# Optimization experiments

Measured on AMD Instinct MI355X. Metric: run time of the kernel, lower is better.

Reference implementation:

```python
import jax, jax.numpy as jnp
import numpy as np

# GConvLSTM (torch_geometric_temporal) single step, H=None,C=None -> zeros.
# Each gate g uses two ChebConvs: conv_x_g(X) + conv_h_g(H) + (w_c_g*C for i,f; only i,f,o have w_c) + b_g
# With H=C=0: gate preact = conv_x_g(X) + conv_h_g(0) + b_g. ChebConv(0)=0 only if bias=False;
# torch_geometric_temporal ChebConvs use bias=True by default, so conv_h_g(0) = bias_h_g (a vector).
# We fold conv_h bias into b. Cheb recursion with sym norm, lambda_max=2 default in ChebConv? Actually
# ChebConv requires lambda_max or normalization='sym' default uses lambda_max=2.0 assumption:
# Tx_0 = x; Tx_1 = L_hat @ x where L_hat = -D^-1/2 A D^-1/2 (since L_scaled = L - I = -A_norm for lambda_max=2);
# Tx_k = 2*L_hat@Tx_{k-1} - Tx_{k-2}. out = sum_k Tx_k @ W_k + bias.

MULT = 2
IN_CH = 10
WIDTHS = [8 * MULT, 16 * MULT, 32 * MULT, 76 * MULT]
KS = [2, 3, 4, 5]
NUM_CLASSES = 2
N_NODES = 100000
N_EDGES = 3200000


def _norm_adj(edge_index, n):
    src, dst = edge_index[0], edge_index[1]
    deg = jax.ops.segment_sum(jnp.ones_like(src, dtype=jnp.float32), dst, num_segments=n)
    dinv = jnp.where(deg > 0, jax.lax.rsqrt(jnp.maximum(deg, 1.0)), 0.0)
    w = dinv[src] * dinv[dst]  # [E]
    return src, dst, w


def _lhat_mul(x, src, dst, w, n):
    # L_hat @ x = -A_norm @ x  (lambda_max=2, sym norm, no self loops added in scaled L beyond -I cancel)
    msg = x[src] * w[:, None]  # [E,F]
    agg = jax.ops.segment_sum(msg, dst, num_segments=n)
    return -agg


def cheb_conv(x, Ws, b, src, dst, w, n):
    # Ws: [K, F_in, F_out]
    K = Ws.shape[0]
    Tx0 = x
    out = Tx0 @ Ws[0]
    if K > 1:
        Tx1 = _lhat_mul(Tx0, src, dst, w, n)
        out = out + Tx1 @ Ws[1]
        for k in range(2, K):
            Tx2 = 2.0 * _lhat_mul(Tx1, src, dst, w, n) - Tx0
            out = out + Tx2 @ Ws[k]
            Tx0, Tx1 = Tx1, Tx2
    return out + b


def gconv_lstm_step(x, params, src, dst, w, n):
    # params: dict with per-gate Wx,Wh (cheb weights), bx,bh, b, and w_ci,w_cf,w_co
    def conv_pair(g):
        cx = cheb_conv(x, params[f'Wx_{g}'], params[f'bx_{g}'], src, dst, w, n)
        # H = 0 => conv_h contributes only its bias
        return cx + params[f'bh_{g}'] + params[f'b_{g}']
    # C = 0 => peephole terms w_c*C vanish
    i = jax.nn.sigmoid(conv_pair('i'))
    f = jax.nn.sigmoid(conv_pair('f'))
    c = i * jnp.tanh(conv_pair('c'))
    o = jax.nn.sigmoid(conv_pair('o'))
    h = o * jnp.tanh(c)
    return h


def _make_layer_params(key, f_in, f_out, K):
    p = {}
    ks = jax.random.split(key, 16)
    scale = 1.0 / np.sqrt(f_in * K)
    for gi, g in enumerate(['i', 'f', 'c', 'o']):
        p[f'Wx_{g}'] = jax.random.normal(ks[4 * gi], (K, f_in, f_out), jnp.float32) * scale
        p[f'bx_{g}'] = jnp.zeros((f_out,), jnp.float32)
        p[f'bh_{g}'] = jnp.zeros((f_out,), jnp.float32)
        p[f'b_{g}'] = jnp.zeros((f_out,), jnp.float32)
    return p


def setup_inputs() -> dict:
    key = jax.random.key(0)
    kx, ke, kp, kl = jax.random.split(key, 4)
    x = jax.random.normal(kx, (N_NODES, IN_CH), jnp.float32)
    edge_index = jax.random.randint(ke, (2, N_EDGES), 0, N_NODES, dtype=jnp.int64)
    layer_keys = jax.random.split(kp, 4)
    params = []
    f_in = IN_CH
    for li, (f_out, K) in enumerate(zip(WIDTHS, KS)):
        params.append(_make_layer_params(layer_keys[li], f_in, f_out, K))
        f_in = f_out
    flat = {}
    for li, p in enumerate(params):
        for k, v in p.items():
            flat[f'l{li}_{k}'] = v
    kw, kb = jax.random.split(kl)
    flat['lin_W'] = jax.random.normal(kw, (WIDTHS[-1], NUM_CLASSES), jnp.float32) * (1.0 / np.sqrt(WIDTHS[-1]))
    flat['lin_b'] = jnp.zeros((NUM_CLASSES,), jnp.float32)
    return {'x': x, 'edge_index': edge_index, **flat}


_GATE_KEYS = [f'{pre}_{g}' for g in ['i', 'f', 'c', 'o'] for pre in ['Wx', 'bx', 'bh', 'b']]


def _forward(x, edge_index, params_by_layer, lin_W, lin_b):
    n = x.shape[0]
    src, dst, w = _norm_adj(edge_index, n)
    h = x
    for p in params_by_layer:
        h = gconv_lstm_step(h, p, src, dst, w, n)
        h = jax.nn.relu(h)  # dropout: eval mode -> identity
    logits = h @ lin_W + lin_b
    return jax.nn.softmax(logits, axis=-1)


def reference(x, edge_index,
              l0_Wx_i, l0_bx_i, l0_bh_i, l0_b_i, l0_Wx_f, l0_bx_f, l0_bh_f, l0_b_f, l0_Wx_c, l0_bx_c, l0_bh_c, l0_b_c, l0_Wx_o, l0_bx_o, l0_bh_o, l0_b_o,
              l1_Wx_i, l1_bx_i, l1_bh_i, l1_b_i, l1_Wx_f, l1_bx_f, l1_bh_f, l1_b_f, l1_Wx_c, l1_bx_c, l1_bh_c, l1_b_c, l1_Wx_o, l1_bx_o, l1_bh_o, l1_b_o,
              l2_Wx_i, l2_bx_i, l2_bh_i, l2_b_i, l2_Wx_f, l2_bx_f, l2_bh_f, l2_b_f, l2_Wx_c, l2_bx_c, l2_bh_c, l2_b_c, l2_Wx_o, l2_bx_o, l2_bh_o, l2_b_o,
              l3_Wx_i, l3_bx_i, l3_bh_i, l3_b_i, l3_Wx_f, l3_bx_f, l3_bh_f, l3_b_f, l3_Wx_c, l3_bx_c, l3_bh_c, l3_b_c, l3_Wx_o, l3_bx_o, l3_bh_o, l3_b_o,
              lin_W, lin_b):
    loc = locals()
    params_by_layer = []
    for li in range(4):
        params_by_layer.append({k: loc[f'l{li}_{k}'] for k in _GATE_KEYS})
    return _forward(x, edge_index, params_by_layer, lin_W, lin_b)
```

## Files before the change

### kernel.cpp

```cpp
#include <hip/hip_runtime.h>


#define IN_CH 10
typedef unsigned short u16;
typedef unsigned long long u64;
typedef short bf16x8 __attribute__((ext_vector_type(8)));
typedef float f32x4 __attribute__((ext_vector_type(4)));

struct __align__(8) Edge { int s; float w; };

__device__ __forceinline__ float bf2f(u16 u) { return __uint_as_float(((unsigned)u) << 16); }
__device__ __forceinline__ float lo16f(unsigned v) { return __uint_as_float(v << 16); }
__device__ __forceinline__ float hi16f(unsigned v) { return __uint_as_float(v & 0xffff0000u); }
__device__ __forceinline__ u16 f2bf(float f) {
    unsigned x = __float_as_uint(f);
    return (u16)((x + 0x7fff + ((x >> 16) & 1)) >> 16);
}
__device__ __forceinline__ float ldv(const float* p) { return *p; }
__device__ __forceinline__ float ldv(const u16* p) { return bf2f(*p); }
__device__ __forceinline__ void stv(float* p, float v) { *p = v; }
__device__ __forceinline__ void stv(u16* p, float v) { *p = f2bf(v); }

__device__ __forceinline__ void gload16(const u16* g, u16* l) {
    __builtin_amdgcn_global_load_lds(
        (const __attribute__((address_space(1))) unsigned*)(const void*)g,
        (__attribute__((address_space(3))) unsigned*)(void*)l, 16, 0, 0);
}


__global__ void k_count(const int* __restrict__ dst, int* __restrict__ cnt, int e) {
    int i = blockIdx.x * 256 + threadIdx.x;
    if (i < e) atomicAdd(&cnt[dst[i]], 1);
}

__global__ void k_dinv(const int* __restrict__ cnt, float* __restrict__ dinv, int n) {
    int i = blockIdx.x * 256 + threadIdx.x;
    if (i < n) dinv[i] = cnt[i] > 0 ? rsqrtf((float)cnt[i]) : 0.f;
}


__global__ void k_bsum(const int* __restrict__ cnt, int* __restrict__ bsum, int n) {
    __shared__ int red[256];
    int t = threadIdx.x;
    int idx = blockIdx.x * 1024 + t * 4;
    int s = 0;
#pragma unroll
    for (int j = 0; j < 4; j++) s += (idx + j < n) ? cnt[idx + j] : 0;
    red[t] = s;
    __syncthreads();
    for (int off = 128; off > 0; off >>= 1) {
        if (t < off) red[t] += red[t + off];
        __syncthreads();
    }
    if (t == 0) bsum[blockIdx.x] = red[0];
}

__global__ __launch_bounds__(1024) void k_bscan(const int* __restrict__ bsum,
                                                int* __restrict__ boff,
                                                int* __restrict__ total_out, int B) {
    __shared__ int sh[1024];
    int t = threadIdx.x;
    int v = t < B ? bsum[t] : 0;
    sh[t] = v;
    __syncthreads();
    for (int off = 1; off < 1024; off <<= 1) {
        int x = (t >= off) ? sh[t - off] : 0;
        __syncthreads();
        sh[t] += x;
        __syncthreads();
    }
    if (t < B) boff[t] = sh[t] - v;
    if (t == B - 1) *total_out = sh[t];
}

__global__ void k_write(const int* __restrict__ cnt, const int* __restrict__ boff,
                        int* __restrict__ row_ptr, int* __restrict__ cursor, int n) {
    __shared__ int tsum[256];
    int t = threadIdx.x;
    int idx = blockIdx.x * 1024 + t * 4;
    int c[4];
    int s = 0;
#pragma unroll
    for (int j = 0; j < 4; j++) {
        c[j] = (idx + j < n) ? cnt[idx + j] : 0;
        s += c[j];
    }
    tsum[t] = s;
    __syncthreads();
    for (int off = 1; off < 256; off <<= 1) {
        int x = (t >= off) ? tsum[t - off] : 0;
        __syncthreads();
        tsum[t] += x;
        __syncthreads();
    }
    int run = boff[blockIdx.x] + tsum[t] - s;
#pragma unroll
    for (int j = 0; j < 4; j++) {
        if (idx + j < n) {
            row_ptr[idx + j] = run;
            cursor[idx + j] = run;
            run += c[j];
        }
    }
}

__global__ void k_fill(const int* __restrict__ src, const int* __restrict__ dst,
                       const float* __restrict__ dinv, int* __restrict__ cursor,
                       Edge* __restrict__ ed, int e, int dlo, int dhi) {
    int i = blockIdx.x * 256 + threadIdx.x;
    if (i >= e) return;
    int d = dst[i];
    if (d < dlo || d >= dhi) return;
    int s = src[i];
    int pos = atomicAdd(&cursor[d], 1);
    float w = dinv[s] * dinv[d];
    u64 v = (u64)(unsigned)s | ((u64)__float_as_uint(w) << 32);
    *(u64*)&ed[pos] = v;
}


template <int F>
__global__ void k_spmv(const u16* __restrict__ X, const u16* __restrict__ Tprev,
                       u16* __restrict__ Tout, const int* __restrict__ row_ptr,
                       const Edge* __restrict__ ed, int n, float scale) {
    int lane = threadIdx.x;
    int node = blockIdx.x * blockDim.y + threadIdx.y;
    if (node >= n) return;
    int lo = row_ptr[node], hi = row_ptr[node + 1];
    const u16* Xc = X + 2 * lane;
    float a0[4] = {0.f, 0.f, 0.f, 0.f};
    float a1[4] = {0.f, 0.f, 0.f, 0.f};
    int e = lo;
    for (; e + 8 <= hi; e += 8) {
        Edge q[8];
#pragma unroll
        for (int j = 0; j < 8; j++) q[j] = ed[e + j];
        unsigned v[8];
#pragma unroll
        for (int j = 0; j < 8; j++)
            v[j] = *(const unsigned*)(Xc + (size_t)q[j].s * F);
#pragma unroll
        for (int j = 0; j < 8; j++) {
            a0[j & 3] = fmaf(q[j].w, lo16f(v[j]), a0[j & 3]);
            a1[j & 3] = fmaf(q[j].w, hi16f(v[j]), a1[j & 3]);
        }
    }
    for (; e + 4 <= hi; e += 4) {
        Edge q[4];
#pragma unroll
        for (int j = 0; j < 4; j++) q[j] = ed[e + j];
        unsigned v[4];
#pragma unroll
        for (int j = 0; j < 4; j++)
            v[j] = *(const unsigned*)(Xc + (size_t)q[j].s * F);
#pragma unroll
        for (int j = 0; j < 4; j++) {
            a0[j] = fmaf(q[j].w, lo16f(v[j]), a0[j]);
            a1[j] = fmaf(q[j].w, hi16f(v[j]), a1[j]);
        }
    }
    for (; e < hi; e++) {
        Edge q = ed[e];
        unsigned v = *(const unsigned*)(Xc + (size_t)q.s * F);
        a0[0] = fmaf(q.w, lo16f(v), a0[0]);
        a1[0] = fmaf(q.w, hi16f(v), a1[0]);
    }
    float v0 = -scale * ((a0[0] + a0[1]) + (a0[2] + a0[3]));
    float v1 = -scale * ((a1[0] + a1[1]) + (a1[2] + a1[3]));
    if (Tprev) {
        unsigned pv = *(const unsigned*)(Tprev + (size_t)node * F + 2 * lane);
        v0 -= lo16f(pv);
        v1 -= hi16f(pv);
    }
    *(unsigned*)(Tout + (size_t)node * F + 2 * lane) =
        (unsigned)f2bf(v0) | ((unsigned)f2bf(v1) << 16);
}

struct TP { const void* p[5]; };

template <typename ST, int FIN, int K>
__global__ __launch_bounds__(256) void k_chebgate(TP tp, const float* __restrict__ Wp,
                                                  const float* __restrict__ b4,
                                                  ST* __restrict__ H, int n, int F,
                                                  int F4pad) {
    __shared__ float As[FIN][68];
    __shared__ float Ws[FIN][128];
    const int tid = threadIdx.x;
    const int fx = tid & 31, ry = tid >> 5;
    const int row0 = blockIdx.y * 64;
    const int f0 = blockIdx.x * 32;
    const int f = f0 + fx;

    float acc[8][3];
    const float4 bv = *(const float4*)&b4[(size_t)f * 4];
#pragma unroll
    for (int r = 0; r < 8; r++) { acc[r][0] = bv.x; acc[r][1] = bv.y; acc[r][2] = bv.z; }

#pragma unroll
    for (int t = 0; t < K; t++) {
        const ST* T = (const ST*)tp.p[t];
        for (int idx = tid; idx < 64 * FIN; idx += 256) {
            int r = idx / FIN, a = idx - r * FIN;
            int rr = row0 + r;
            if (rr >= n) rr = n - 1;
            As[a][r] = ldv(&T[(size_t)rr * FIN + a]);
        }
        const float* Wt = Wp + (size_t)t * FIN * F4pad + (size_t)f0 * 4;
        for (int idx = tid; idx < FIN * 128; idx += 256) {
            int aa = idx >> 7, c = idx & 127;
            Ws[aa][c] = Wt[(size_t)aa * F4pad + c];
        }
        __syncthreads();
#pragma unroll 2
        for (int a = 0; a < FIN; a++) {
            const float4 w = *(const float4*)&Ws[a][fx * 4];
            const float4 x0 = *(const float4*)&As[a][ry * 8];
            const float4 x1 = *(const float4*)&As[a][ry * 8 + 4];
            const float xr[8] = {x0.x, x0.y, x0.z, x0.w, x1.x, x1.y, x1.z, x1.w};
#pragma unroll
            for (int r = 0; r < 8; r++) {
                acc[r][0] = fmaf(xr[r], w.x, acc[r][0]);
                acc[r][1] = fmaf(xr[r], w.y, acc[r][1]);
                acc[r][2] = fmaf(xr[r], w.z, acc[r][2]);
            }
        }
        __syncthreads();
    }

    if (f < F) {
#pragma unroll
        for (int r = 0; r < 8; r++) {
            int row = row0 + ry * 8 + r;
            if (row < n) {
                float gi = 1.f / (1.f + __expf(-acc[r][0]));
                float go = 1.f / (1.f + __expf(-acc[r][2]));
                float c = gi * tanhf(acc[r][1]);
                float h = go * tanhf(c);
                stv(&H[(size_t)row * F + f], fmaxf(h, 0.f));
            }
        }
    }
}


template <int FIN, int K, int NT, int FPAD>
__global__ __launch_bounds__(256) void k_chebgate_mfma2(TP tp, const u16* __restrict__ Bp,
                                                        const float* __restrict__ b3,
                                                        u16* __restrict__ H, int n, int F,
                                                        int Hstride) {
    constexpr int NIT = K * FIN / 32;
    constexpr int CPR = FIN / 8;
    constexpr int CSH = (CPR == 8) ? 3 : 2;
    constexpr int PANEL = 128 * FIN;
    constexpr int IPT = (128 * CPR) / 256;
    __shared__ __align__(16) u16 Alds[K * PANEL];

    const int tid = threadIdx.x;
    const int xb = blockIdx.x;
    const int wv = tid >> 6, lane = tid & 63;
    const int ln = lane & 15, lk = lane >> 4;
    const size_t panel_g = (size_t)xb * 128 * FIN;

#pragma unroll
    for (int t = 0; t < K; t++) {
        const u16* g = (const u16*)tp.p[t] + panel_g;
#pragma unroll
        for (int i = 0; i < IPT; i++) {
            int j0 = wv * (IPT * 64) + i * 64;
            int j = j0 + lane;
            int row = j >> CSH, c = j & (CPR - 1);
            int sc = (j & ~(CPR - 1)) | (c ^ (row & (CPR - 1)));
            gload16(g + (size_t)sc * 8, Alds + (size_t)t * PANEL + (size_t)j0 * 8);
        }
    }
    __syncthreads();

    const int r0 = xb * 128 + wv * 32;
    const u16* Bl = Bp + (size_t)lane * 8;

#pragma unroll 1
    for (int yb = 0; yb < NT; yb++) {
        f32x4 acc[2][2][3];
#pragma unroll
        for (int rt = 0; rt < 2; rt++)
#pragma unroll
            for (int s = 0; s < 2; s++)
#pragma unroll
                for (int g = 0; g < 3; g++) acc[rt][s][g] = (f32x4){0.f, 0.f, 0.f, 0.f};

#pragma unroll
        for (int it = 0; it < NIT; it++) {
            const int k0 = it * 32;
            const int t = k0 / FIN;
            const int a0 = k0 % FIN;
            bf16x8 af[2];
#pragma unroll
            for (int rt = 0; rt < 2; rt++) {
                int lrow = wv * 32 + rt * 16 + ln;
                int kc = (a0 >> 3) + lk;
                int kcs = kc ^ (lrow & (CPR - 1));
                af[rt] = *(const bf16x8*)(Alds + (size_t)t * PANEL + (size_t)lrow * FIN + kcs * 8);
            }
#pragma unroll
            for (int s = 0; s < 2; s++)
#pragma unroll
                for (int g = 0; g < 3; g++) {
                    int fi = (yb * NIT + it) * 6 + s * 3 + g;
                    bf16x8 bf = *(const bf16x8*)(Bl + (size_t)fi * 512);
#pragma unroll
                    for (int rt = 0; rt < 2; rt++)
                        acc[rt][s][g] = __builtin_amdgcn_mfma_f32_16x16x32_bf16(
                            af[rt], bf, acc[rt][s][g], 0, 0, 0);
                }
        }

        const int f0 = yb * 32;
#pragma unroll
        for (int s = 0; s < 2; s++) {
            int fcol = f0 + s * 16 + ln;
            if (fcol >= F) continue;
            float bi = b3[0 * FPAD + fcol];
            float bc = b3[1 * FPAD + fcol];
            float bo = b3[2 * FPAD + fcol];
#pragma unroll
            for (int rt = 0; rt < 2; rt++) {
#pragma unroll
                for (int reg = 0; reg < 4; reg++) {
                    int row = r0 + rt * 16 + lk * 4 + reg;
                    if (row < n) {
                        float gi = 1.f / (1.f + __expf(-(acc[rt][s][0][reg] + bi)));
                        float go = 1.f / (1.f + __expf(-(acc[rt][s][2][reg] + bo)));
                        float c = gi * tanhf(acc[rt][s][1][reg] + bc);
                        float h = go * tanhf(c);
                        H[(size_t)row * Hstride + fcol] = f2bf(fmaxf(h, 0.f));
                    }
                }
            }
        }
    }
}


template <int FIN, int K, int NT, int FPAD>
__global__ __launch_bounds__(256) void k_chebgate_mfma_fused2(
    TP tp, const u16* __restrict__ Bp, const float* __restrict__ b3,
    const float* __restrict__ W2, float* __restrict__ part, int n, int F) {
    constexpr int NIT = K * FIN / 32;
    constexpr int CPR = FIN / 8;
    constexpr int CSH = (CPR == 8) ? 3 : 2;
    constexpr int PANEL = 128 * FIN;
    constexpr int IPT = (128 * CPR) / 256;
    __shared__ __align__(16) u16 Alds[K * PANEL];

    const int tid = threadIdx.x;
    const int xb = blockIdx.x;
    const int wv = tid >> 6, lane = tid & 63;
    const int ln = lane & 15, lk = lane >> 4;
    const size_t panel_g = (size_t)xb * 128 * FIN;

#pragma unroll
    for (int t = 0; t < K; t++) {
        const u16* g = (const u16*)tp.p[t] + panel_g;
#pragma unroll
        for (int i = 0; i < IPT; i++) {
            int j0 = wv * (IPT * 64) + i * 64;
            int j = j0 + lane;
            int row = j >> CSH, c = j & (CPR - 1);
            int sc = (j & ~(CPR - 1)) | (c ^ (row & (CPR - 1)));
            gload16(g + (size_t)sc * 8, Alds + (size_t)t * PANEL + (size_t)j0 * 8);
        }
    }
    __syncthreads();

    const int r0 = xb * 128 + wv * 32;
    const u16* Bl = Bp + (size_t)lane * 8;

#pragma unroll 1
    for (int yb = 0; yb < NT; yb++) {
        f32x4 acc[2][2][3];
#pragma unroll
        for (int rt = 0; rt < 2; rt++)
#pragma unroll
            for (int s = 0; s < 2; s++)
#pragma unroll
                for (int g = 0; g < 3; g++) acc[rt][s][g] = (f32x4){0.f, 0.f, 0.f, 0.f};

#pragma unroll
        for (int it = 0; it < NIT; it++) {
            const int k0 = it * 32;
            const int t = k0 / FIN;
            const int a0 = k0 % FIN;
            bf16x8 af[2];
#pragma unroll
            for (int rt = 0; rt < 2; rt++) {
                int lrow = wv * 32 + rt * 16 + ln;
                int kc = (a0 >> 3) + lk;
                int kcs = kc ^ (lrow & (CPR - 1));
                af[rt] = *(const bf16x8*)(Alds + (size_t)t * PANEL + (size_t)lrow * FIN + kcs * 8);
            }
#pragma unroll
            for (int s = 0; s < 2; s++)
#pragma unroll
                for (int g = 0; g < 3; g++) {
                    int fi = (yb * NIT + it) * 6 + s * 3 + g;
                    bf16x8 bf = *(const bf16x8*)(Bl + (size_t)fi * 512);
#pragma unroll
                    for (int rt = 0; rt < 2; rt++)
                        acc[rt][s][g] = __builtin_amdgcn_mfma_f32_16x16x32_bf16(
                            af[rt], bf, acc[rt][s][g], 0, 0, 0);
                }
        }

        const int f0 = yb * 32;
        float p0[2][4], p1[2][4];
#pragma unroll
        for (int rt = 0; rt < 2; rt++)
#pragma unroll
            for (int reg = 0; reg < 4; reg++) { p0[rt][reg] = 0.f; p1[rt][reg] = 0.f; }

#pragma unroll
        for (int s = 0; s < 2; s++) {
            int fcol = f0 + s * 16 + ln;
            float w20 = fcol < F ? W2[fcol * 2 + 0] : 0.f;
            float w21 = fcol < F ? W2[fcol * 2 + 1] : 0.f;
            float bi = b3[0 * FPAD + fcol];
            float bc = b3[1 * FPAD + fcol];
            float bo = b3[2 * FPAD + fcol];
#pragma unroll
            for (int rt = 0; rt < 2; rt++) {
#pragma unroll
                for (int reg = 0; reg < 4; reg++) {
                    float gi = 1.f / (1.f + __expf(-(acc[rt][s][0][reg] + bi)));
                    float go = 1.f / (1.f + __expf(-(acc[rt][s][2][reg] + bo)));
                    float c = gi * tanhf(acc[rt][s][1][reg] + bc);
                    float h = fmaxf(go * tanhf(c), 0.f);
                    p0[rt][reg] = fmaf(h, w20, p0[rt][reg]);
                    p1[rt][reg] = fmaf(h, w21, p1[rt][reg]);
                }
            }
        }

#pragma unroll
        for (int rt = 0; rt < 2; rt++) {
#pragma unroll
            for (int reg = 0; reg < 4; reg++) {
                float v0 = p0[rt][reg], v1 = p1[rt][reg];
#pragma unroll
                for (int m = 1; m <= 8; m <<= 1) {
                    v0 += __shfl_xor(v0, m);
                    v1 += __shfl_xor(v1, m);
                }
                p0[rt][reg] = v0;
                p1[rt][reg] = v1;
            }
        }

        if (ln == 0) {
#pragma unroll
            for (int rt = 0; rt < 2; rt++) {
#pragma unroll
                for (int reg = 0; reg < 4; reg++) {
                    int row = r0 + rt * 16 + lk * 4 + reg;
                    if (row < n) {
                        float* pp = part + ((size_t)yb * n + row) * 2;
                        pp[0] = p0[rt][reg];
                        pp[1] = p1[rt][reg];
                    }
                }
            }
        }
    }
}

__global__ void k_smax(const float* __restrict__ part, const float* __restrict__ b,
                       float* __restrict__ out, int n, int ntiles) {
    int i = blockIdx.x * 256 + threadIdx.x;
    if (i >= n) return;
    float l0 = b[0], l1 = b[1];
    for (int t = 0; t < ntiles; t++) {
        const float* pp = part + ((size_t)t * n + i) * 2;
        l0 += pp[0];
        l1 += pp[1];
    }
    float m = fmaxf(l0, l1);
    float e0 = __expf(l0 - m), e1 = __expf(l1 - m);
    float s = 1.f / (e0 + e1);
    out[(size_t)i * 2 + 0] = e0 * s;
    out[(size_t)i * 2 + 1] = e1 * s;
}


__global__ void k_pack_w(const float* __restrict__ Wi, const float* __restrict__ Wc,
                         const float* __restrict__ Wo, float* __restrict__ Wp,
                         int KFIN, int F, int F4pad) {
    int idx = blockIdx.x * 256 + threadIdx.x;
    int tot = KFIN * F4pad;
    if (idx >= tot) return;
    int c = idx % F4pad;
    int ka = idx / F4pad;
    int f = c >> 2, g = c & 3;
    float v = 0.f;
    if (g < 3 && f < F) {
        const float* Wg = (g == 0) ? Wi : ((g == 1) ? Wc : Wo);
        v = Wg[(size_t)ka * F + f];
    }
    Wp[idx] = v;
}

__global__ void k_pack_b(const float* __restrict__ bxi, const float* __restrict__ bhi,
                         const float* __restrict__ bi, const float* __restrict__ bxc,
                         const float* __restrict__ bhc, const float* __restrict__ bc,
                         const float* __restrict__ bxo, const float* __restrict__ bho,
                         const float* __restrict__ bo, float* __restrict__ b4,
                         int F, int F4pad) {
    int idx = blockIdx.x * 256 + threadIdx.x;
    if (idx >= F4pad) return;
    int f = idx >> 2, g = idx & 3;
    float v = 0.f;
    if (g < 3 && f < F) {
        if (g == 0) v = bxi[f] + bhi[f] + bi[f];
        else if (g == 1) v = bxc[f] + bhc[f] + bc[f];
        else v = bxo[f] + bho[f] + bo[f];
    }
    b4[idx] = v;
}

__global__ void k_pack_wf(const float* __restrict__ Wi, const float* __restrict__ Wc,
                          const float* __restrict__ Wo, u16* __restrict__ Bp,
                          int NIT, int Fin, int F, int NT) {
    int idx = blockIdx.x * 256 + threadIdx.x;
    int tot = NT * NIT * 6 * 512;
    if (idx >= tot) return;
    int frag = idx >> 9;
    int r = idx & 511;
    int lane = r >> 3, j = r & 7;
    int lk = lane >> 4, ln = lane & 15;
    int yb = frag / (NIT * 6);
    int q = frag % (NIT * 6);
    int it = q / 6, sg = q % 6;
    int s = sg / 3, g = sg % 3;
    int fcol = yb * 32 + s * 16 + ln;
    int k = it * 32 + lk * 8 + j;
    int t = k / Fin, a = k % Fin;
    float v = 0.f;
    if (fcol < F) {
        const float* Wg = (g == 0) ? Wi : ((g == 1) ? Wc : Wo);
        v = Wg[((size_t)t * Fin + a) * F + fcol];
    }
    Bp[idx] = f2bf(v);
}

__global__ void k_pack_b3(const float* __restrict__ bxi, const float* __restrict__ bhi,
                          const float* __restrict__ bi, const float* __restrict__ bxc,
                          const float* __restrict__ bhc, const float* __restrict__ bc,
                          const float* __restrict__ bxo, const float* __restrict__ bho,
                          const float* __restrict__ bo, float* __restrict__ b3,
                          int F, int FPAD) {
    int idx = blockIdx.x * 256 + threadIdx.x;
    if (idx >= 3 * FPAD) return;
    int g = idx / FPAD, f = idx % FPAD;
    float v = 0.f;
    if (f < F) {
        if (g == 0) v = bxi[f] + bhi[f] + bi[f];
        else if (g == 1) v = bxc[f] + bhc[f] + bc[f];
        else v = bxo[f] + bho[f] + bo[f];
    }
    b3[idx] = v;
}

__global__ void k_cvt(const float* __restrict__ x, u16* __restrict__ y, int n) {
    int i = blockIdx.x * 256 + threadIdx.x;
    if (i < n) y[i] = f2bf(x[i]);
}


static inline size_t al(size_t x) { return (x + 255) & ~(size_t)255; }

extern "C" void kernel_launch(void* const* d_in, const int* in_sizes, int n_in,
                              void* d_out, int out_size, void* d_ws, size_t ws_size,
                              hipStream_t stream) {
    const float* X0 = (const float*)d_in[0];
    const int* ei = (const int*)d_in[1];
    const int N = in_sizes[0] / IN_CH;
    const int E = in_sizes[1] / 2;
    const int* src = ei;
    const int* dst = ei + E;

    char* p = (char*)d_ws;
    size_t off = 0;
    auto carve = [&](size_t bytes) -> char* { char* r = p + off; off += al(bytes); return r; };
    int* row_ptr  = (int*)carve((size_t)(N + 1) * 4);
    int* cnt      = (int*)carve((size_t)N * 4);
    int* cursor   = (int*)carve((size_t)N * 4);
    float* dinv   = (float*)carve((size_t)N * 4);
    int* bsum     = (int*)carve((size_t)1024 * 4);
    int* boff     = (int*)carve((size_t)1024 * 4);
    Edge* edges   = (Edge*)carve((size_t)E * 8);
    const size_t S64 = al((size_t)N * 64 * 2);
    char* bufA    = carve(5 * S64);
    char* bufB    = carve((size_t)N * 304);
    float* Wp     = (float*)carve((size_t)48 * 128 * 4);
    float* b4     = (float*)carve((size_t)128 * 4);
    u16* Wt       = (u16*)carve((size_t)480 * 320 * 2);
    float* b3     = (float*)carve((size_t)480 * 4);
    (void)ws_size;

    u16* X0c  = (u16*)bufA;
    u16* T0_1 = (u16*)(bufA + al((size_t)N * 20));
    u16* H0   = (u16*)(bufA + S64);
    u16* T1_1 = (u16*)(bufA + S64 + al((size_t)N * 32));
    u16* T1_2 = (u16*)(bufA + S64 + 2 * al((size_t)N * 32));
    u16* L2T[4];
    for (int t = 0; t < 4; t++) L2T[t] = (u16*)(bufB + t * al((size_t)N * 64));
    u16* L3T[5];
    for (int t = 0; t < 5; t++) L3T[t] = (u16*)(bufA + t * S64);
    float* part = (float*)bufB;

    int gE = (E + 255) / 256, gN = (N + 255) / 256;
    int B = (N + 1023) / 1024;
    hipMemsetAsync(cnt, 0, (size_t)N * 4, stream);
    k_count<<<gE, 256, 0, stream>>>(dst, cnt, E);
    k_dinv<<<gN, 256, 0, stream>>>(cnt, dinv, N);
    k_bsum<<<B, 256, 0, stream>>>(cnt, bsum, N);
    k_bscan<<<1, 1024, 0, stream>>>(bsum, boff, row_ptr + N, B);
    k_write<<<B, 256, 0, stream>>>(cnt, boff, row_ptr, cursor, N);
    const int NB = 8;
    for (int b = 0; b < NB; b++) {
        int dlo = (int)((long long)N * b / NB);
        int dhi = (int)((long long)N * (b + 1) / NB);
        k_fill<<<gE, 256, 0, stream>>>(src, dst, dinv, cursor, edges, E, dlo, dhi);
    }

    k_cvt<<<(N * IN_CH + 255) / 256, 256, 0, stream>>>(X0, X0c, N * IN_CH);

    dim3 gv(1, (N + 63) / 64);
    int rb = (N + 127) / 128;

    dim3 bs5(5, 48);   int g5 = (N + 47) / 48;
    dim3 bs8(8, 32);   int g8 = (N + 31) / 32;
    dim3 bs16(16, 16); int g16 = (N + 15) / 16;
    dim3 bs32(32, 8);  int g32 = (N + 7) / 8;

    {
        k_pack_w<<<(20 * 128 + 255) / 256, 256, 0, stream>>>(
            (const float*)d_in[2], (const float*)d_in[10], (const float*)d_in[14], Wp, 20, 16, 128);
        k_pack_b<<<1, 256, 0, stream>>>(
            (const float*)d_in[3], (const float*)d_in[4], (const float*)d_in[5],
            (const float*)d_in[11], (const float*)d_in[12], (const float*)d_in[13],
            (const float*)d_in[15], (const float*)d_in[16], (const float*)d_in[17], b4, 16, 128);
        k_spmv<10><<<g5, bs5, 0, stream>>>(X0c, nullptr, T0_1, row_ptr, edges, N, 1.f);
        TP tp; tp.p[0] = X0c; tp.p[1] = T0_1;
        k_chebgate<u16, 10, 2><<<gv, 256, 0, stream>>>(tp, Wp, b4, H0, N, 16, 128);
    }
    {
        k_pack_w<<<(48 * 128 + 255) / 256, 256, 0, stream>>>(
            (const float*)d_in[18], (const float*)d_in[26], (const float*)d_in[30], Wp, 48, 32, 128);
        k_pack_b<<<1, 256, 0, stream>>>(
            (const float*)d_in[19], (const float*)d_in[20], (const float*)d_in[21],
            (const float*)d_in[27], (const float*)d_in[28], (const float*)d_in[29],
            (const float*)d_in[31], (const float*)d_in[32], (const float*)d_in[33], b4, 32, 128);
        k_spmv<16><<<g8, bs8, 0, stream>>>(H0, nullptr, T1_1, row_ptr, edges, N, 1.f);
        k_spmv<16><<<g8, bs8, 0, stream>>>(T1_1, H0, T1_2, row_ptr, edges, N, 2.f);
        TP tp; tp.p[0] = H0; tp.p[1] = T1_1; tp.p[2] = T1_2;
        k_chebgate<u16, 16, 3><<<gv, 256, 0, stream>>>(tp, Wp, b4, L2T[0], N, 32, 128);
    }
    {
        k_pack_wf<<<(2 * 4 * 6 * 512 + 255) / 256, 256, 0, stream>>>(
            (const float*)d_in[34], (const float*)d_in[42], (const float*)d_in[46], Wt, 4, 32, 64, 2);
        k_pack_b3<<<1, 256, 0, stream>>>(
            (const float*)d_in[35], (const float*)d_in[36], (const float*)d_in[37],
            (const float*)d_in[43], (const float*)d_in[44], (const float*)d_in[45],
            (const float*)d_in[47], (const float*)d_in[48], (const float*)d_in[49], b3, 64, 64);
        k_spmv<32><<<g16, bs16, 0, stream>>>(L2T[0], nullptr, L2T[1], row_ptr, edges, N, 1.f);
        k_spmv<32><<<g16, bs16, 0, stream>>>(L2T[1], L2T[0], L2T[2], row_ptr, edges, N, 2.f);
        k_spmv<32><<<g16, bs16, 0, stream>>>(L2T[2], L2T[1], L2T[3], row_ptr, edges, N, 2.f);
        TP tp; for (int t = 0; t < 4; t++) tp.p[t] = L2T[t];
        k_chebgate_mfma2<32, 4, 2, 64><<<rb, 256, 0, stream>>>(tp, Wt, b3, L3T[0], N, 64, 64);
    }
    {
        k_pack_wf<<<(5 * 10 * 6 * 512 + 255) / 256, 256, 0, stream>>>(
            (const float*)d_in[50], (const float*)d_in[58], (const float*)d_in[62], Wt, 10, 64, 152, 5);
        k_pack_b3<<<2, 256, 0, stream>>>(
            (const float*)d_in[51], (const float*)d_in[52], (const float*)d_in[53],
            (const float*)d_in[59], (const float*)d_in[60], (const float*)d_in[61],
            (const float*)d_in[63], (const float*)d_in[64], (const float*)d_in[65], b3, 152, 160);
        k_spmv<64><<<g32, bs32, 0, stream>>>(L3T[0], nullptr, L3T[1], row_ptr, edges, N, 1.f);
        k_spmv<64><<<g32, bs32, 0, stream>>>(L3T[1], L3T[0], L3T[2], row_ptr, edges, N, 2.f);
        k_spmv<64><<<g32, bs32, 0, stream>>>(L3T[2], L3T[1], L3T[3], row_ptr, edges, N, 2.f);
        k_spmv<64><<<g32, bs32, 0, stream>>>(L3T[3], L3T[2], L3T[4], row_ptr, edges, N, 2.f);
        TP tp; for (int t = 0; t < 5; t++) tp.p[t] = L3T[t];
        k_chebgate_mfma_fused2<64, 5, 5, 160><<<rb, 256, 0, stream>>>(
            tp, Wt, b3, (const float*)d_in[66], part, N, 152);
    }

    k_smax<<<gN, 256, 0, stream>>>(part, (const float*)d_in[67], (float*)d_out, N, 5);
}
```

Measured before the change: 1.182 ms.

## Build CSR with LDS-privatized per-bucket histograms and scatter cursors

Replaces the global-atomic degree count and the eight-pass global-atomic fill with a two-level scheme. Each of 64 edge partitions builds a shared-memory histogram for each of 8 destination buckets of 12800 nodes. The per-partition counts are summed and turned into per-partition cursor seeds, so the scatter step only does atomics in LDS. This targets contention and traffic from global atomics, at the cost of an 8x re-read of the dst array, a 64x-node histogram buffer in workspace, and a 51KB LDS footprint per block. BUKN*NBUK is hardcoded to cover 100000 nodes.

```diff
diff --git a/kernel.cpp b/kernel.cpp
--- a/kernel.cpp
+++ b/kernel.cpp
@@ -2,6 +2,9 @@
 
 
 #define IN_CH 10
+#define NBUK 8
+#define PBLK 64
+#define BUKN 12800
 typedef unsigned short u16;
 typedef unsigned long long u64;
 typedef short bf16x8 __attribute__((ext_vector_type(8)));
@@ -28,9 +31,76 @@
 }
 
 
-__global__ void k_count(const int* __restrict__ dst, int* __restrict__ cnt, int e) {
-    int i = blockIdx.x * 256 + threadIdx.x;
-    if (i < e) atomicAdd(&cnt[dst[i]], 1);
+__global__ __launch_bounds__(256) void k_hist8(const int* __restrict__ dst,
+                                               int* __restrict__ H, int e, int n) {
+    __shared__ int sh[BUKN];
+    const int p = blockIdx.x, b = blockIdx.y;
+    const int lo = b * BUKN;
+    const int hi = min(lo + BUKN, n);
+    const int cl = hi - lo;
+    for (int i = threadIdx.x; i < cl; i += 256) sh[i] = 0;
+    __syncthreads();
+    const int chunk = (e + PBLK - 1) / PBLK;
+    const int e0 = p * chunk, e1 = min(e0 + chunk, e);
+    for (int i = e0 + threadIdx.x; i < e1; i += 256) {
+        int d = dst[i];
+        if (d >= lo && d < hi) atomicAdd(&sh[d - lo], 1);
+    }
+    __syncthreads();
+    int* Hb = H + (size_t)(b * PBLK + p) * BUKN;
+    for (int i = threadIdx.x; i < cl; i += 256) Hb[i] = sh[i];
+}
+
+__global__ void k_hsum(const int* __restrict__ H, int* __restrict__ cnt, int n) {
+    int t = blockIdx.x * 256 + threadIdx.x;
+    if (t >= n) return;
+    int b = t / BUKN, ln = t % BUKN;
+    const int* Hb = H + (size_t)b * PBLK * BUKN + ln;
+    int s = 0;
+#pragma unroll 8
+    for (int p = 0; p < PBLK; p++) s += Hb[(size_t)p * BUKN];
+    cnt[t] = s;
+}
+
+__global__ void k_cseed(int* __restrict__ H, const int* __restrict__ row_ptr, int n) {
+    int t = blockIdx.x * 256 + threadIdx.x;
+    if (t >= n) return;
+    int b = t / BUKN, ln = t % BUKN;
+    int* Hb = H + (size_t)b * PBLK * BUKN + ln;
+    int run = row_ptr[t];
+#pragma unroll 4
+    for (int p = 0; p < PBLK; p++) {
+        int v = Hb[(size_t)p * BUKN];
+        Hb[(size_t)p * BUKN] = run;
+        run += v;
+    }
+}
+
+__global__ __launch_bounds__(256) void k_scatter(const int* __restrict__ src,
+                                                 const int* __restrict__ dst,
+                                                 const float* __restrict__ dinv,
+                                                 const int* __restrict__ H,
+                                                 Edge* __restrict__ ed, int e, int n) {
+    __shared__ int cur[BUKN];
+    const int p = blockIdx.x, b = blockIdx.y;
+    const int lo = b * BUKN;
+    const int hi = min(lo + BUKN, n);
+    const int cl = hi - lo;
+    const int* Cb = H + (size_t)(b * PBLK + p) * BUKN;
+    for (int i = threadIdx.x; i < cl; i += 256) cur[i] = Cb[i];
+    __syncthreads();
+    const int chunk = (e + PBLK - 1) / PBLK;
+    const int e0 = p * chunk, e1 = min(e0 + chunk, e);
+    for (int i = e0 + threadIdx.x; i < e1; i += 256) {
+        int d = dst[i];
+        if (d >= lo && d < hi) {
+            int s = src[i];
+            int pos = atomicAdd(&cur[d - lo], 1);
+            float w = dinv[s] * dinv[d];
+            u64 v = (u64)(unsigned)s | ((u64)__float_as_uint(w) << 32);
+            *(u64*)&ed[pos] = v;
+        }
+    }
 }
 
 __global__ void k_dinv(const int* __restrict__ cnt, float* __restrict__ dinv, int n) {
@@ -102,20 +172,6 @@
             run += c[j];
         }
     }
-}
-
-__global__ void k_fill(const int* __restrict__ src, const int* __restrict__ dst,
-                       const float* __restrict__ dinv, int* __restrict__ cursor,
-                       Edge* __restrict__ ed, int e, int dlo, int dhi) {
-    int i = blockIdx.x * 256 + threadIdx.x;
-    if (i >= e) return;
-    int d = dst[i];
-    if (d < dlo || d >= dhi) return;
-    int s = src[i];
-    int pos = atomicAdd(&cursor[d], 1);
-    float w = dinv[s] * dinv[d];
-    u64 v = (u64)(unsigned)s | ((u64)__float_as_uint(w) << 32);
-    *(u64*)&ed[pos] = v;
 }
 
 
@@ -615,21 +671,19 @@
     u16* L3T[5];
     for (int t = 0; t < 5; t++) L3T[t] = (u16*)(bufA + t * S64);
     float* part = (float*)bufB;
-
-    int gE = (E + 255) / 256, gN = (N + 255) / 256;
+    int* Hh = (int*)bufB;
+
+    int gN = (N + 255) / 256;
     int B = (N + 1023) / 1024;
-    hipMemsetAsync(cnt, 0, (size_t)N * 4, stream);
-    k_count<<<gE, 256, 0, stream>>>(dst, cnt, E);
+    dim3 gh(PBLK, NBUK);
+    k_hist8<<<gh, 256, 0, stream>>>(dst, Hh, E, N);
+    k_hsum<<<gN, 256, 0, stream>>>(Hh, cnt, N);
     k_dinv<<<gN, 256, 0, stream>>>(cnt, dinv, N);
     k_bsum<<<B, 256, 0, stream>>>(cnt, bsum, N);
     k_bscan<<<1, 1024, 0, stream>>>(bsum, boff, row_ptr + N, B);
     k_write<<<B, 256, 0, stream>>>(cnt, boff, row_ptr, cursor, N);
-    const int NB = 8;
-    for (int b = 0; b < NB; b++) {
-        int dlo = (int)((long long)N * b / NB);
-        int dhi = (int)((long long)N * (b + 1) / NB);
-        k_fill<<<gE, 256, 0, stream>>>(src, dst, dinv, cursor, edges, E, dlo, dhi);
-    }
+    k_cseed<<<gN, 256, 0, stream>>>(Hh, row_ptr, N);
+    k_scatter<<<gh, 256, 0, stream>>>(src, dst, dinv, Hh, edges, E, N);
 
     k_cvt<<<(N * IN_CH + 255) / 256, 256, 0, stream>>>(X0, X0c, N * IN_CH);
 
```

Measured after the change: 1.081 ms. 8.6% less time.

## Build CSR via two-level bucketed counting sort with shared-memory atomics

Applied to the files above, without the earlier changes.

Replaces the global-atomic degree count and the eight-pass filtered fill with a two-level radix-style bucket sort. Edges are first partitioned by destination bucket (dst>>8) using per-block shared-memory histograms and a prefix scan, staged into temporary arrays, then each bucket block counts per-node degrees and scatters edges with shared-memory cursors. This removes repeated full passes over the edge list and contended global atomics, in exchange for extra staging traffic in a reused buffer and more kernel launches. Edge order within a row becomes nondeterministic, which only affects floating-point summation order.

```diff
diff --git a/kernel.cpp b/kernel.cpp
--- a/kernel.cpp
+++ b/kernel.cpp
@@ -2,6 +2,8 @@
 
 
 #define IN_CH 10
+#define PCH 128
+#define NB2MAX 512
 typedef unsigned short u16;
 typedef unsigned long long u64;
 typedef short bf16x8 __attribute__((ext_vector_type(8)));
@@ -28,9 +30,103 @@
 }
 
 
-__global__ void k_count(const int* __restrict__ dst, int* __restrict__ cnt, int e) {
-    int i = blockIdx.x * 256 + threadIdx.x;
-    if (i < e) atomicAdd(&cnt[dst[i]], 1);
+__global__ __launch_bounds__(256) void k_bcount(const int* __restrict__ dst,
+                                                int* __restrict__ C, int e, int nb2) {
+    __shared__ int sh[NB2MAX];
+    const int p = blockIdx.x;
+    for (int i = threadIdx.x; i < nb2; i += 256) sh[i] = 0;
+    __syncthreads();
+    const int chunk = (e + PCH - 1) / PCH;
+    const int e0 = p * chunk, e1 = min(e0 + chunk, e);
+    for (int i = e0 + threadIdx.x; i < e1; i += 256)
+        atomicAdd(&sh[dst[i] >> 8], 1);
+    __syncthreads();
+    for (int b = threadIdx.x; b < nb2; b += 256) C[b * PCH + p] = sh[b];
+}
+
+__global__ __launch_bounds__(512) void k_boff(int* __restrict__ C, int* __restrict__ seg,
+                                              int nb2) {
+    __shared__ int sh[512];
+    const int t = threadIdx.x;
+    int tot = 0;
+    if (t < nb2) {
+        int* Cb = C + (size_t)t * PCH;
+        int run = 0;
+#pragma unroll 4
+        for (int p = 0; p < PCH; p++) { int v = Cb[p]; Cb[p] = run; run += v; }
+        tot = run;
+    }
+    sh[t] = tot;
+    __syncthreads();
+    for (int off = 1; off < 512; off <<= 1) {
+        int x = (t >= off) ? sh[t - off] : 0;
+        __syncthreads();
+        sh[t] += x;
+        __syncthreads();
+    }
+    const int base = sh[t] - tot;
+    if (t < nb2) {
+        seg[t] = base;
+        int* Cb = C + (size_t)t * PCH;
+#pragma unroll 4
+        for (int p = 0; p < PCH; p++) Cb[p] += base;
+        if (t == nb2 - 1) seg[nb2] = base + tot;
+    }
+}
+
+__global__ __launch_bounds__(256) void k_stage(const int* __restrict__ src,
+                                               const int* __restrict__ dst,
+                                               const int* __restrict__ C,
+                                               int* __restrict__ Sd, int* __restrict__ Ss,
+                                               int e, int nb2) {
+    __shared__ int cur[NB2MAX];
+    const int p = blockIdx.x;
+    for (int i = threadIdx.x; i < nb2; i += 256) cur[i] = C[(size_t)i * PCH + p];
+    __syncthreads();
+    const int chunk = (e + PCH - 1) / PCH;
+    const int e0 = p * chunk, e1 = min(e0 + chunk, e);
+    for (int i = e0 + threadIdx.x; i < e1; i += 256) {
+        int d = dst[i], s = src[i];
+        int pos = atomicAdd(&cur[d >> 8], 1);
+        Sd[pos] = d;
+        Ss[pos] = s;
+    }
+}
+
+__global__ __launch_bounds__(256) void k_bknt(const int* __restrict__ Sd,
+                                              const int* __restrict__ seg,
+                                              int* __restrict__ cnt, int n) {
+    __shared__ int sh[256];
+    const int b = blockIdx.x;
+    sh[threadIdx.x] = 0;
+    __syncthreads();
+    const int lo = seg[b], hi = seg[b + 1];
+    for (int i = lo + threadIdx.x; i < hi; i += 256)
+        atomicAdd(&sh[Sd[i] & 255], 1);
+    __syncthreads();
+    int node = b * 256 + threadIdx.x;
+    if (node < n) cnt[node] = sh[threadIdx.x];
+}
+
+__global__ __launch_bounds__(256) void k_bscat(const int* __restrict__ Sd,
+                                               const int* __restrict__ Ss,
+                                               const int* __restrict__ seg,
+                                               const int* __restrict__ row_ptr,
+                                               const float* __restrict__ dinv,
+                                               Edge* __restrict__ ed, int n) {
+    __shared__ int cur[256];
+    const int b = blockIdx.x;
+    int node = b * 256 + threadIdx.x;
+    cur[threadIdx.x] = node < n ? row_ptr[node] : 0;
+    __syncthreads();
+    const int lo = seg[b], hi = seg[b + 1];
+    for (int i = lo + threadIdx.x; i < hi; i += 256) {
+        int d = Sd[i], s = Ss[i];
+        int pos = atomicAdd(&cur[d & 255], 1);
+        float w = dinv[s] * dinv[d];
+        u64 v = (u64)(unsigned)s | ((u64)__float_as_uint(w) << 32);
+        *(u64*)&ed[pos] = v;
+    }
 }
 
 __global__ void k_dinv(const int* __restrict__ cnt, float* __restrict__ dinv, int n) {
@@ -102,20 +198,6 @@
             run += c[j];
         }
     }
-}
-
-__global__ void k_fill(const int* __restrict__ src, const int* __restrict__ dst,
-                       const float* __restrict__ dinv, int* __restrict__ cursor,
-                       Edge* __restrict__ ed, int e, int dlo, int dhi) {
-    int i = blockIdx.x * 256 + threadIdx.x;
-    if (i >= e) return;
-    int d = dst[i];
-    if (d < dlo || d >= dhi) return;
-    int s = src[i];
-    int pos = atomicAdd(&cursor[d], 1);
-    float w = dinv[s] * dinv[d];
-    u64 v = (u64)(unsigned)s | ((u64)__float_as_uint(w) << 32);
-    *(u64*)&ed[pos] = v;
 }
 
 
@@ -595,6 +677,8 @@
     float* dinv   = (float*)carve((size_t)N * 4);
     int* bsum     = (int*)carve((size_t)1024 * 4);
     int* boff     = (int*)carve((size_t)1024 * 4);
+    int* Cb       = (int*)carve((size_t)NB2MAX * PCH * 4);
+    int* seg      = (int*)carve((size_t)(NB2MAX + 1) * 4);
     Edge* edges   = (Edge*)carve((size_t)E * 8);
     const size_t S64 = al((size_t)N * 64 * 2);
     char* bufA    = carve(5 * S64);
@@ -615,21 +699,21 @@
     u16* L3T[5];
     for (int t = 0; t < 5; t++) L3T[t] = (u16*)(bufA + t * S64);
     float* part = (float*)bufB;
-
-    int gE = (E + 255) / 256, gN = (N + 255) / 256;
+    int* Sd = (int*)bufA;
+    int* Ss = (int*)(bufA + al((size_t)E * 4));
+
+    int gN = (N + 255) / 256;
     int B = (N + 1023) / 1024;
-    hipMemsetAsync(cnt, 0, (size_t)N * 4, stream);
-    k_count<<<gE, 256, 0, stream>>>(dst, cnt, E);
+    int nb2 = (N + 255) / 256;
+    k_bcount<<<PCH, 256, 0, stream>>>(dst, Cb, E, nb2);
+    k_boff<<<1, 512, 0, stream>>>(Cb, seg, nb2);
+    k_stage<<<PCH, 256, 0, stream>>>(src, dst, Cb, Sd, Ss, E, nb2);
+    k_bknt<<<nb2, 256, 0, stream>>>(Sd, seg, cnt, N);
     k_dinv<<<gN, 256, 0, stream>>>(cnt, dinv, N);
     k_bsum<<<B, 256, 0, stream>>>(cnt, bsum, N);
     k_bscan<<<1, 1024, 0, stream>>>(bsum, boff, row_ptr + N, B);
     k_write<<<B, 256, 0, stream>>>(cnt, boff, row_ptr, cursor, N);
-    const int NB = 8;
-    for (int b = 0; b < NB; b++) {
-        int dlo = (int)((long long)N * b / NB);
-        int dhi = (int)((long long)N * (b + 1) / NB);
-        k_fill<<<gE, 256, 0, stream>>>(src, dst, dinv, cursor, edges, E, dlo, dhi);
-    }
+    k_bscat<<<nb2, 256, 0, stream>>>(Sd, Ss, seg, row_ptr, dinv, edges, N);
 
     k_cvt<<<(N * IN_CH + 255) / 256, 256, 0, stream>>>(X0, X0c, N * IN_CH);
 
```

Result: faster. 1.033 ms (-12.6%).
